# Optimization experiments

Measured on AMD Instinct MI355X. Metric: run time of the kernel, lower is better.

The kernel has to match this reference:

```python
import jax, jax.numpy as jnp
import numpy as np

B, NA, NB = 2, 2048, 2048
DIM_A, DIM_B = 256, 256
HEADS, DH_A, DH_B = 8, 64, 64
INNER_A, INNER_B = DH_A * HEADS, DH_B * HEADS
EPS = 1e-5


def layer_norm(x, w, b):
    m = jnp.mean(x, axis=-1, keepdims=True)
    v = jnp.mean(jnp.square(x - m), axis=-1, keepdims=True)
    return (x - m) * jax.lax.rsqrt(v + EPS) * w + b


def setup_inputs() -> dict:
    key = jax.random.key(0)
    ks = jax.random.split(key, 16)
    s = 0.02
    return {
        "feat_a": jax.random.normal(ks[0], (B, NA, DIM_A), jnp.float32),
        "feat_b": jax.random.normal(ks[1], (B, NB, DIM_B), jnp.float32),
        "mask_a_b": jax.random.bernoulli(ks[2], 0.5, (B, NA, NB)),
        # linear weights stored (in, out)
        "Wq": jax.random.normal(ks[3], (DIM_A, INNER_B), jnp.float32) * s,
        "bq": jnp.zeros((INNER_B,), jnp.float32),
        "Wk": jax.random.normal(ks[4], (DIM_B, INNER_B), jnp.float32) * s,
        "bk": jnp.zeros((INNER_B,), jnp.float32),
        "Wv": jax.random.normal(ks[5], (DIM_B, INNER_A), jnp.float32) * s,
        "bv": jnp.zeros((INNER_A,), jnp.float32),
        "Wg": jax.random.normal(ks[6], (DIM_A, INNER_A), jnp.float32) * s,
        "bg": jnp.zeros((INNER_A,), jnp.float32),
        "Wo": jax.random.normal(ks[7], (INNER_A, DIM_A), jnp.float32) * s,
        "bo": jnp.zeros((DIM_A,), jnp.float32),
        "ln_a_w": jnp.ones((DIM_A,), jnp.float32),
        "ln_a_b": jnp.zeros((DIM_A,), jnp.float32),
        "ln_b_w": jnp.ones((DIM_B,), jnp.float32),
        "ln_b_b": jnp.zeros((DIM_B,), jnp.float32),
        "qln_w": jnp.ones((INNER_B,), jnp.float32),
        "qln_b": jnp.zeros((INNER_B,), jnp.float32),
        "kln_w": jnp.ones((INNER_B,), jnp.float32),
        "kln_b": jnp.zeros((INNER_B,), jnp.float32),
    }


def reference(feat_a, feat_b, mask_a_b, Wq, bq, Wk, bk, Wv, bv, Wg, bg, Wo, bo,
              ln_a_w, ln_a_b, ln_b_w, ln_b_b, qln_w, qln_b, kln_w, kln_b):
    scale = DH_B ** -0.5
    fa = layer_norm(feat_a, ln_a_w, ln_a_b)            # (b, na, dim_a)
    fb = layer_norm(feat_b, ln_b_w, ln_b_b)            # (b, nb, dim_b)
    q = layer_norm(fa @ Wq + bq, qln_w, qln_b)         # (b, na, inner_b)
    k = layer_norm(fb @ Wk + bk, kln_w, kln_b)         # (b, nb, inner_b)
    v = fb @ Wv + bv                                   # (b, nb, inner_a)
    g = fa @ Wg + bg                                   # (b, na, inner_a)
    q = q.reshape(B, NA, HEADS, DH_B)
    k = k.reshape(B, NB, HEADS, DH_B)
    v = v.reshape(B, NB, HEADS, DH_A)
    g = g.reshape(B, NA, HEADS, DH_A)
    sim = jnp.einsum('bihd,bjhd->bhij', q, k) * scale  # (b, h, na, nb)
    neg = jnp.finfo(sim.dtype).min
    sim = jnp.where(mask_a_b[:, None, :, :], sim, neg)
    attn = jax.nn.softmax(sim, axis=-1)
    out = jnp.einsum('bhij,bjhd->bihd', attn, v)       # (b, na, h, dh_a)
    out = jax.nn.sigmoid(g) * out
    out = out.reshape(B, NA, INNER_A)
    return out @ Wo + bo                               # (b, na, dim_a)
```

## Files before the change

kernel.cpp:

```cpp
#include <hip/hip_runtime.h>
#include <hip/hip_bf16.h>

using bf16 = __hip_bfloat16;
typedef short bf16x8 __attribute__((ext_vector_type(8)));
typedef float f32x4 __attribute__((ext_vector_type(4)));
typedef unsigned short ushort8_t __attribute__((ext_vector_type(8)));
typedef unsigned long long u64;

static constexpr int NA_ = 2048, NB_ = 2048;
static constexpr int H_ = 8, DH_ = 64, INNER_ = 512;
static constexpr int MROWS = 2 * NA_;

#define MFMA32(a, b, c) __builtin_amdgcn_mfma_f32_16x16x32_bf16(a, b, c, 0, 0, 0)

__device__ __forceinline__ unsigned short bfbits(float x) {
  bf16 h = __float2bfloat16(x);
  return __builtin_bit_cast(unsigned short, h);
}
__device__ __forceinline__ float b2f(unsigned short u) {
  unsigned v = ((unsigned)u) << 16;
  return __builtin_bit_cast(float, v);
}

__global__ __launch_bounds__(256) void prep_kernel(
    const float* __restrict__ fa_in, const float* __restrict__ fb_in,
    const float* __restrict__ law, const float* __restrict__ lab,
    const float* __restrict__ lbw, const float* __restrict__ lbb,
    bf16* __restrict__ fa, bf16* __restrict__ fb,
    const float* __restrict__ Wq, const float* __restrict__ Wk,
    const float* __restrict__ Wv, const float* __restrict__ Wg,
    const float* __restrict__ Wo,
    bf16* __restrict__ Wqt, bf16* __restrict__ Wkt,
    bf16* __restrict__ Wvt, bf16* __restrict__ Wgt,
    bf16* __restrict__ Woth, bf16* __restrict__ Wotl,
    const void* __restrict__ maskp, u64* __restrict__ mbits) {
  int blk = blockIdx.x;
  int t = threadIdx.x;
  if (blk < 2048) {
    int row = blk * 4 + (t >> 6);
    int lane = t & 63;
    const float *src, *w, *bb;
    bf16* dst;
    int r;
    if (row < MROWS) { src = fa_in; w = law; bb = lab; dst = fa; r = row; }
    else             { src = fb_in; w = lbw; bb = lbb; dst = fb; r = row - MROWS; }
    float4 x = *(const float4*)(src + (size_t)r * 256 + lane * 4);
    float s  = (x.x + x.y) + (x.z + x.w);
    float s2 = (x.x * x.x + x.y * x.y) + (x.z * x.z + x.w * x.w);
#pragma unroll
    for (int m = 32; m >= 1; m >>= 1) { s += __shfl_xor(s, m); s2 += __shfl_xor(s2, m); }
    float mean = s * (1.0f / 256.0f);
    float var  = s2 * (1.0f / 256.0f) - mean * mean;
    float rstd = rsqrtf(var + 1e-5f);
    float4 wv = *(const float4*)(w + lane * 4);
    float4 bv = *(const float4*)(bb + lane * 4);
    ushort4 o;
    o.x = bfbits((x.x - mean) * rstd * wv.x + bv.x);
    o.y = bfbits((x.y - mean) * rstd * wv.y + bv.y);
    o.z = bfbits((x.z - mean) * rstd * wv.z + bv.z);
    o.w = bfbits((x.w - mean) * rstd * wv.w + bv.w);
    *(ushort4*)(dst + (size_t)r * 256 + lane * 4) = o;
  } else if (blk < 4608) {
    int z = (blk - 2048) >> 9;
    int idx = ((blk - 2048) & 511) * 256 + t;
    if (z < 4) {
      const float* W = (z == 0) ? Wq : (z == 1) ? Wk : (z == 2) ? Wv : Wg;
      bf16* Wt = (z == 0) ? Wqt : (z == 1) ? Wkt : (z == 2) ? Wvt : Wgt;
      int kk = idx >> 9, n = idx & 511;
      Wt[n * 256 + kk] = __float2bfloat16(W[idx]);
    } else {
      int kk = idx >> 8, n = idx & 255;
      float w = Wo[idx];
      bf16 hi = __float2bfloat16(w);
      Woth[n * 512 + kk] = hi;
      Wotl[n * 512 + kk] = __float2bfloat16(w - __bfloat162float(hi));
    }
  } else {
    __shared__ unsigned shf[4];
    const unsigned char* mu = (const unsigned char*)maskp;
    bool nz = ((t & 3) != 0) && (mu[t] != 0);
    u64 bal = __ballot(nz);
    if ((t & 63) == 0) shf[t >> 6] = (bal != 0ull) ? 1u : 0u;
    __syncthreads();
    bool m8 = (shf[0] | shf[1] | shf[2] | shf[3]) != 0;
    int lane = t & 63, wid = t >> 6;
    int lb = blk - 4608;
    for (size_t word = (size_t)lb * 4 + wid; word < 131072; word += 8192) {
      size_t e = word * 64 + lane;
      int v = m8 ? (int)mu[e] : ((const int*)maskp)[e];
      u64 b2 = __ballot(v != 0);
      if (lane == 0) mbits[word] = b2;
    }
  }
}

__global__ __launch_bounds__(256) void gemm4_kernel(
    const bf16* __restrict__ fa, const bf16* __restrict__ fb,
    const bf16* __restrict__ Wqt, const bf16* __restrict__ Wkt,
    const bf16* __restrict__ Wgt, const bf16* __restrict__ Wvt,
    const float* __restrict__ bq, const float* __restrict__ bk,
    const float* __restrict__ bg, const float* __restrict__ bv,
    const float* __restrict__ qlw, const float* __restrict__ qlb,
    const float* __restrict__ klw, const float* __restrict__ klb,
    bf16* __restrict__ qo, bf16* __restrict__ ko,
    bf16* __restrict__ gout, bf16* __restrict__ vout) {
  __shared__ __align__(16) char sm[27648];
  int z = blockIdx.z;
  int t = threadIdx.x, wave = t >> 6, lane = t & 63;
  int lm = lane & 15, quad = lane >> 4, q8 = quad * 8;

  if (z < 2) {
    bf16* As = (bf16*)sm;
    float* Pred = (float*)(sm + 16896);
    float* MV   = (float*)(sm + 17408);
    const bf16* A    = z ? fb : fa;
    const bf16* Wt   = z ? Wkt : Wqt;
    const float* bias = z ? bk : bq;
    const float* lw  = z ? klw : qlw;
    const float* lb  = z ? klb : qlb;
    bf16* out        = z ? ko : qo;
    int m0 = blockIdx.x * 16;
#pragma unroll
    for (int i = 0; i < 2; i++) {
      int id = t + 256 * i, r = id >> 5, cg = id & 31;
      *(ushort8_t*)(&As[r * 264 + cg * 8]) =
          *(const ushort8_t*)(A + (size_t)(m0 + r) * 256 + cg * 8);
    }
    __syncthreads();
    int n0w = wave * 128;
    f32x4 acc[8] = {};
    const bf16* wrow[8];
#pragma unroll
    for (int ni = 0; ni < 8; ni++) wrow[ni] = Wt + (size_t)(n0w + ni * 16 + lm) * 256;
#pragma unroll
    for (int ks = 0; ks < 8; ks++) {
      int k0 = ks * 32;
      bf16x8 af = *(const bf16x8*)(&As[lm * 264 + k0 + q8]);
#pragma unroll
      for (int ni = 0; ni < 8; ni++) {
        bf16x8 bf_ = *(const bf16x8*)(wrow[ni] + k0 + q8);
        acc[ni] = MFMA32(af, bf_, acc[ni]);
      }
    }
    float bvv[8];
#pragma unroll
    for (int ni = 0; ni < 8; ni++) bvv[ni] = bias[n0w + ni * 16 + lm];
#pragma unroll
    for (int ni = 0; ni < 8; ni++)
#pragma unroll
      for (int r = 0; r < 4; r++) acc[ni][r] += bvv[ni];
#pragma unroll
    for (int r = 0; r < 4; r++) {
      float s = 0.f, s2 = 0.f;
#pragma unroll
      for (int ni = 0; ni < 8; ni++) { s += acc[ni][r]; s2 += acc[ni][r] * acc[ni][r]; }
#pragma unroll
      for (int m = 1; m <= 8; m <<= 1) { s += __shfl_xor(s, m); s2 += __shfl_xor(s2, m); }
      if (lm == 0) {
        int row = quad * 4 + r;
        Pred[row * 8 + wave * 2]     = s;
        Pred[row * 8 + wave * 2 + 1] = s2;
      }
    }
    __syncthreads();
    if (t < 16) {
      float s = 0.f, s2 = 0.f;
#pragma unroll
      for (int w = 0; w < 4; w++) { s += Pred[t * 8 + w * 2]; s2 += Pred[t * 8 + w * 2 + 1]; }
      float mean = s * (1.0f / 512.0f);
      float var  = s2 * (1.0f / 512.0f) - mean * mean;
      MV[t * 2]     = mean;
      MV[t * 2 + 1] = rsqrtf(var + 1e-5f);
    }
    __syncthreads();
    float lww[8], lbb_[8];
#pragma unroll
    for (int ni = 0; ni < 8; ni++) {
      lww[ni]  = lw[n0w + ni * 16 + lm];
      lbb_[ni] = lb[n0w + ni * 16 + lm];
    }
#pragma unroll
    for (int r = 0; r < 4; r++) {
      int row = quad * 4 + r;
      float mean = MV[row * 2], rstd = MV[row * 2 + 1];
      size_t obase = (size_t)(m0 + row) * 512 + n0w;
#pragma unroll
      for (int ni = 0; ni < 8; ni++)
        out[obase + ni * 16 + lm] =
            __float2bfloat16((acc[ni][r] - mean) * rstd * lww[ni] + lbb_[ni]);
    }
  } else {
    bf16* As = (bf16*)sm;
    bf16* Bs = (bf16*)(sm + 18432);
    const bf16* A    = (z == 3) ? fb : fa;
    const bf16* Wt   = (z == 3) ? Wvt : Wgt;
    const float* bias = (z == 3) ? bv : bg;
    int x = blockIdx.x;
    int m0 = (x >> 3) * 128, n0 = (x & 7) * 64;
    int wm = wave * 32;
    f32x4 acc[2][4] = {};
    for (int k0 = 0; k0 < 256; k0 += 64) {
      __syncthreads();
#pragma unroll
      for (int i = 0; i < 4; i++) {
        int id = t + 256 * i, r = id >> 3, cg = id & 7;
        *(ushort8_t*)(&As[r * 72 + cg * 8]) =
            *(const ushort8_t*)(A + (size_t)(m0 + r) * 256 + k0 + cg * 8);
      }
#pragma unroll
      for (int i = 0; i < 2; i++) {
        int id = t + 256 * i, r = id >> 3, cg = id & 7;
        *(ushort8_t*)(&Bs[r * 72 + cg * 8]) =
            *(const ushort8_t*)(Wt + (size_t)(n0 + r) * 256 + k0 + cg * 8);
      }
      __syncthreads();
#pragma unroll
      for (int kk = 0; kk < 64; kk += 32) {
        bf16x8 af[2], bf_[4];
#pragma unroll
        for (int mi = 0; mi < 2; mi++)
          af[mi] = *(const bf16x8*)(&As[(wm + mi * 16 + lm) * 72 + kk + q8]);
#pragma unroll
        for (int ni = 0; ni < 4; ni++)
          bf_[ni] = *(const bf16x8*)(&Bs[(ni * 16 + lm) * 72 + kk + q8]);
#pragma unroll
        for (int mi = 0; mi < 2; mi++)
#pragma unroll
          for (int ni = 0; ni < 4; ni++)
            acc[mi][ni] = MFMA32(af[mi], bf_[ni], acc[mi][ni]);
      }
    }
    if (z == 2) {
#pragma unroll
      for (int mi = 0; mi < 2; mi++)
#pragma unroll
        for (int ni = 0; ni < 4; ni++) {
          int nn = n0 + ni * 16 + lm;
          float bvv = bias[nn];
          int mb = m0 + wm + mi * 16 + quad * 4;
#pragma unroll
          for (int r = 0; r < 4; r++)
            gout[(size_t)(mb + r) * 512 + nn] = __float2bfloat16(acc[mi][ni][r] + bvv);
        }
    } else {
      __syncthreads();
      bf16* buf = (bf16*)sm;
#pragma unroll
      for (int mi = 0; mi < 2; mi++)
#pragma unroll
        for (int ni = 0; ni < 4; ni++) {
          int d_local = ni * 16 + lm;
          float bvv = bias[n0 + d_local];
          int j_local = wm + mi * 16 + quad * 4;
#pragma unroll
          for (int r = 0; r < 4; r++)
            buf[d_local * 136 + j_local + r] = __float2bfloat16(acc[mi][ni][r] + bvv);
        }
      __syncthreads();
      int bidx2 = m0 >> 11, j0g = m0 & 2047, hh = n0 >> 6;
      int dl = t >> 2, jseg = (t & 3) * 32;
      bf16* dstrow = vout + (size_t)((bidx2 * 8 + hh) * 64 + dl) * 2048 + j0g + jseg;
#pragma unroll
      for (int c = 0; c < 4; c++)
        *(ushort8_t*)(dstrow + c * 8) = *(const ushort8_t*)(&buf[dl * 136 + jseg + c * 8]);
    }
  }
}

__global__ __launch_bounds__(512) void attn_kernel(
    const bf16* __restrict__ q, const bf16* __restrict__ k,
    const bf16* __restrict__ vt, const bf16* __restrict__ g,
    const u64* __restrict__ mbits,
    bf16* __restrict__ gh, bf16* __restrict__ gl) {
  __shared__ __align__(16) char smem[65024];
  bf16* Qs = (bf16*)smem;
  bf16* KsB = (bf16*)(smem + 9216);
  bf16* VsB = (bf16*)(smem + 27648);
  bf16* PsB = (bf16*)(smem + 46080);
  float* Om = (float*)(smem + 9216);
  float* Lbuf = (float*)(smem + 64512);

  int qt = blockIdx.x, bh = blockIdx.y;
  int bidx = bh >> 3, h = bh & 7;
  int i0 = qt * 64;
  int t = threadIdx.x, wave = t >> 6, lane = t & 63;
  int jhalf = wave >> 2, w4 = wave & 3;
  int lm = lane & 15, quad = lane >> 4, q8 = quad * 8;
  int lt = t & 255;
  int sr0 = lt >> 3, scg = (lt & 7) * 8;

  {
    int r = t >> 3, cg = t & 7;
    *(ushort8_t*)(&Qs[r * 72 + cg * 8]) =
        *(const ushort8_t*)(q + (size_t)(bidx * NA_ + i0 + r) * INNER_ + h * DH_ + cg * 8);
  }
  __syncthreads();
  bf16x8 bq0 = *(const bf16x8*)(&Qs[(w4 * 16 + lm) * 72 + q8]);
  bf16x8 bq1 = *(const bf16x8*)(&Qs[(w4 * 16 + lm) * 72 + 32 + q8]);

  f32x4 oacc[4] = {};
  float psum = 0.f;
  const float scale2 = 0.125f * 1.44269504088896f;

  const bf16* kb = k + (size_t)(bidx * NB_) * INNER_ + h * DH_;
  const bf16* vb = vt + (size_t)(bh * DH_) * NB_;
  bf16* Pw = PsB + wave * (16 * 72);
  bf16* Ks = KsB + jhalf * (64 * 72);
  bf16* Vs = VsB + jhalf * (64 * 72);
  const u64* mrp = mbits + ((size_t)(bidx * NA_ + i0 + w4 * 16 + lm)) * (NB_ / 64) + jhalf * 16;

  const bf16* ksrc0 = kb + (size_t)(jhalf * 1024 + sr0) * INNER_ + scg;
  const bf16* ksrc1 = kb + (size_t)(jhalf * 1024 + sr0 + 32) * INNER_ + scg;
  const bf16* vsrc0 = vb + (size_t)sr0 * NB_ + jhalf * 1024 + scg;
  const bf16* vsrc1 = vb + (size_t)(sr0 + 32) * NB_ + jhalf * 1024 + scg;

  ushort8_t kr0, kr1, vr0, vr1;
  kr0 = *(const ushort8_t*)(ksrc0);
  kr1 = *(const ushort8_t*)(ksrc1);
  vr0 = *(const ushort8_t*)(vsrc0);
  vr1 = *(const ushort8_t*)(vsrc1);
  u64 smw = mrp[0] >> (quad * 4);

  for (int it = 0; it < 16; it++) {
    __syncthreads();
    *(ushort8_t*)(&Ks[sr0 * 72 + scg])        = kr0;
    *(ushort8_t*)(&Ks[(sr0 + 32) * 72 + scg]) = kr1;
    *(ushort8_t*)(&Vs[sr0 * 72 + scg])        = vr0;
    *(ushort8_t*)(&Vs[(sr0 + 32) * 72 + scg]) = vr1;
    __syncthreads();

    u64 nsm = smw;
    if (it < 15) {
      int joff = (it + 1) * 64;
      kr0 = *(const ushort8_t*)(ksrc0 + (size_t)joff * INNER_);
      kr1 = *(const ushort8_t*)(ksrc1 + (size_t)joff * INNER_);
      vr0 = *(const ushort8_t*)(vsrc0 + joff);
      vr1 = *(const ushort8_t*)(vsrc1 + joff);
      nsm = mrp[it + 1] >> (quad * 4);
    }

    f32x4 st[4];
#pragma unroll
    for (int nt = 0; nt < 4; nt++) {
      bf16x8 a0 = *(const bf16x8*)(&Ks[(nt * 16 + lm) * 72 + q8]);
      bf16x8 a1 = *(const bf16x8*)(&Ks[(nt * 16 + lm) * 72 + 32 + q8]);
      f32x4 a = {0.f, 0.f, 0.f, 0.f};
      a = MFMA32(a0, bq0, a);
      a = MFMA32(a1, bq1, a);
      st[nt] = a;
    }

    float pr[4][4];
#pragma unroll
    for (int nt = 0; nt < 4; nt++)
#pragma unroll
      for (int r = 0; r < 4; r++) {
        float p = exp2f(st[nt][r] * scale2);
        unsigned live = (unsigned)(smw >> (nt * 16 + r)) & 1u;
        pr[nt][r] = live ? p : 0.0f;
      }

    float s0 = (pr[0][0] + pr[0][1]) + (pr[0][2] + pr[0][3]);
    float s1 = (pr[1][0] + pr[1][1]) + (pr[1][2] + pr[1][3]);
    float s2 = (pr[2][0] + pr[2][1]) + (pr[2][2] + pr[2][3]);
    float s3 = (pr[3][0] + pr[3][1]) + (pr[3][2] + pr[3][3]);
    psum += (s0 + s1) + (s2 + s3);

#pragma unroll
    for (int nt = 0; nt < 4; nt++) {
      ushort4 pk;
      pk.x = bfbits(pr[nt][0]);
      pk.y = bfbits(pr[nt][1]);
      pk.z = bfbits(pr[nt][2]);
      pk.w = bfbits(pr[nt][3]);
      *(ushort4*)(Pw + lm * 72 + nt * 16 + quad * 4) = pk;
    }

    bf16x8 ap0 = *(const bf16x8*)(&Pw[lm * 72 + q8]);
    bf16x8 ap1 = *(const bf16x8*)(&Pw[lm * 72 + 32 + q8]);
#pragma unroll
    for (int c = 0; c < 4; c++) {
      bf16x8 v0 = *(const bf16x8*)(&Vs[(c * 16 + lm) * 72 + q8]);
      bf16x8 v1 = *(const bf16x8*)(&Vs[(c * 16 + lm) * 72 + 32 + q8]);
      oacc[c] = MFMA32(ap0, v0, oacc[c]);
      oacc[c] = MFMA32(ap1, v1, oacc[c]);
    }
    smw = nsm;
  }

  psum += __shfl_xor(psum, 16);
  psum += __shfl_xor(psum, 32);

  __syncthreads();
  if (quad == 0) Lbuf[jhalf * 64 + w4 * 16 + lm] = psum;
  if (jhalf == 1) {
#pragma unroll
    for (int c = 0; c < 4; c++)
#pragma unroll
      for (int r = 0; r < 4; r++)
        Om[w4 * (16 * 66) + (quad * 4 + r) * 66 + c * 16 + lm] = oacc[c][r];
  }
  __syncthreads();
  if (jhalf == 0) {
    int mrow = i0 + w4 * 16 + quad * 4;
    float inv[4];
#pragma unroll
    for (int r = 0; r < 4; r++) {
      float l = Lbuf[w4 * 16 + quad * 4 + r] + Lbuf[64 + w4 * 16 + quad * 4 + r];
      inv[r] = 1.0f / l;
    }
#pragma unroll
    for (int c = 0; c < 4; c++) {
      int col = h * DH_ + c * 16 + lm;
#pragma unroll
      for (int r = 0; r < 4; r++) {
        float o = oacc[c][r] + Om[w4 * (16 * 66) + (quad * 4 + r) * 66 + c * 16 + lm];
        size_t idx = (size_t)(bidx * NA_ + mrow + r) * INNER_ + col;
        float gv = b2f(__builtin_bit_cast(unsigned short, g[idx]));
        float sig = 1.0f / (1.0f + __expf(-gv));
        float val = o * inv[r] * sig;
        unsigned short hb = bfbits(val);
        gh[idx] = __builtin_bit_cast(bf16, hb);
        gl[idx] = __float2bfloat16(val - b2f(hb));
      }
    }
  }
}

__global__ __launch_bounds__(256) void gemm_split_kernel(
    const bf16* __restrict__ Ah, const bf16* __restrict__ Al,
    const bf16* __restrict__ Bh, const bf16* __restrict__ Bl,
    const float* __restrict__ bias, float* __restrict__ C) {
  constexpr int K = 512, N = 256;
  __shared__ __align__(16) bf16 Ash[32 * 72];
  __shared__ __align__(16) bf16 Asl[32 * 72];
  __shared__ __align__(16) bf16 Bsh[64 * 72];
  __shared__ __align__(16) bf16 Bsl[64 * 72];
  int n0 = blockIdx.x * 64, m0 = blockIdx.y * 32;
  int t = threadIdx.x, wave = t >> 6, lane = t & 63;
  int lm = lane & 15, quad = lane >> 4, q8 = quad * 8;
  int wm = (wave & 1) * 16, wn = (wave >> 1) * 32;
  f32x4 acc[2] = {};
  for (int k0 = 0; k0 < K; k0 += 64) {
    __syncthreads();
    {
      int r = t >> 3, cg = t & 7;
      size_t ga = (size_t)(m0 + r) * K + k0 + cg * 8;
      *(ushort8_t*)(&Ash[r * 72 + cg * 8]) = *(const ushort8_t*)(Ah + ga);
      *(ushort8_t*)(&Asl[r * 72 + cg * 8]) = *(const ushort8_t*)(Al + ga);
    }
#pragma unroll
    for (int i = 0; i < 2; i++) {
      int id = t + 256 * i, r = id >> 3, cg = id & 7;
      size_t gb = (size_t)(n0 + r) * K + k0 + cg * 8;
      *(ushort8_t*)(&Bsh[r * 72 + cg * 8]) = *(const ushort8_t*)(Bh + gb);
      *(ushort8_t*)(&Bsl[r * 72 + cg * 8]) = *(const ushort8_t*)(Bl + gb);
    }
    __syncthreads();
#pragma unroll
    for (int kk = 0; kk < 64; kk += 32) {
      bf16x8 ah = *(const bf16x8*)(&Ash[(wm + lm) * 72 + kk + q8]);
      bf16x8 al = *(const bf16x8*)(&Asl[(wm + lm) * 72 + kk + q8]);
#pragma unroll
      for (int ni = 0; ni < 2; ni++) {
        bf16x8 bh_ = *(const bf16x8*)(&Bsh[(wn + ni * 16 + lm) * 72 + kk + q8]);
        bf16x8 bl_ = *(const bf16x8*)(&Bsl[(wn + ni * 16 + lm) * 72 + kk + q8]);
        acc[ni] = MFMA32(ah, bh_, acc[ni]);
        acc[ni] = MFMA32(ah, bl_, acc[ni]);
        acc[ni] = MFMA32(al, bh_, acc[ni]);
      }
    }
  }
#pragma unroll
  for (int ni = 0; ni < 2; ni++) {
    int n = n0 + wn + ni * 16 + lm;
    float bvv = bias[n];
    int mb = m0 + wm + quad * 4;
#pragma unroll
    for (int r = 0; r < 4; r++) C[(size_t)(mb + r) * N + n] = acc[ni][r] + bvv;
  }
}

extern "C" void kernel_launch(void* const* d_in, const int* in_sizes, int n_in,
                              void* d_out, int out_size, void* d_ws, size_t ws_size,
                              hipStream_t stream) {
  const float* feat_a = (const float*)d_in[0];
  const float* feat_b = (const float*)d_in[1];
  const void*  mask   = d_in[2];
  const float* Wq = (const float*)d_in[3];
  const float* bq = (const float*)d_in[4];
  const float* Wk = (const float*)d_in[5];
  const float* bk = (const float*)d_in[6];
  const float* Wv = (const float*)d_in[7];
  const float* bv = (const float*)d_in[8];
  const float* Wg = (const float*)d_in[9];
  const float* bg = (const float*)d_in[10];
  const float* Wo = (const float*)d_in[11];
  const float* bo = (const float*)d_in[12];
  const float* law = (const float*)d_in[13];
  const float* lab = (const float*)d_in[14];
  const float* lbw = (const float*)d_in[15];
  const float* lbb = (const float*)d_in[16];
  const float* qlw = (const float*)d_in[17];
  const float* qlb = (const float*)d_in[18];
  const float* klw = (const float*)d_in[19];
  const float* klb = (const float*)d_in[20];

  char* ws = (char*)d_ws;
  size_t off = 0;
  auto alloc = [&](size_t bytes) -> void* {
    void* p = ws + off;
    off += (bytes + 255) & ~(size_t)255;
    return p;
  };
  bf16* fa    = (bf16*)alloc((size_t)MROWS * 256 * 2);
  bf16* fb    = (bf16*)alloc((size_t)MROWS * 256 * 2);
  bf16* Wqt   = (bf16*)alloc((size_t)131072 * 2);
  bf16* Wkt   = (bf16*)alloc((size_t)131072 * 2);
  bf16* Wvt   = (bf16*)alloc((size_t)131072 * 2);
  bf16* Wgt   = (bf16*)alloc((size_t)131072 * 2);
  bf16* Woth  = (bf16*)alloc((size_t)131072 * 2);
  bf16* Wotl  = (bf16*)alloc((size_t)131072 * 2);
  bf16* qb_   = (bf16*)alloc((size_t)MROWS * 512 * 2);
  bf16* kb_   = (bf16*)alloc((size_t)MROWS * 512 * 2);
  bf16* vtb   = (bf16*)alloc((size_t)1024 * 2048 * 2);
  bf16* gbuf  = (bf16*)alloc((size_t)MROWS * 512 * 2);
  bf16* gh    = (bf16*)alloc((size_t)MROWS * 512 * 2);
  bf16* gl    = (bf16*)alloc((size_t)MROWS * 512 * 2);
  u64*  mbits = (u64*)alloc((size_t)131072 * 8);

  prep_kernel<<<6656, 256, 0, stream>>>(
      feat_a, feat_b, law, lab, lbw, lbb, fa, fb,
      Wq, Wk, Wv, Wg, Wo, Wqt, Wkt, Wvt, Wgt, Woth, Wotl, mask, mbits);
  gemm4_kernel<<<dim3(256, 1, 4), 256, 0, stream>>>(
      fa, fb, Wqt, Wkt, Wgt, Wvt, bq, bk, bg, bv,
      qlw, qlb, klw, klb, qb_, kb_, gbuf, vtb);
  attn_kernel<<<dim3(32, 16), 512, 0, stream>>>(qb_, kb_, vtb, gbuf, mbits, gh, gl);
  gemm_split_kernel<<<dim3(4, 128), 256, 0, stream>>>(gh, gl, Woth, Wotl, bo, (float*)d_out);
}
```

Measured before the change: 202.1 us.

## Fold softmax scale into q LayerNorm and compute row sums via MFMA

Folds the attention scale and log2e factor into the q LayerNorm weight and bias, which removes a multiply per score. Masked scores are set to -200 before a raw hardware exp2, replacing the exp-then-select sequence. Probabilities are packed to bf16 with an add-and-permute round instead of the library conversion. Row sums now come from an extra pair of MFMAs against a ones vector rather than scalar adds and shuffles. The row sums now use bf16-rounded probabilities, and pkbf's simplified rounding (ties not handled to even) differs slightly from the library conversion.

```diff
diff --git a/kernel.cpp b/kernel.cpp
--- a/kernel.cpp
+++ b/kernel.cpp
@@ -13,6 +13,12 @@
 
 #define MFMA32(a, b, c) __builtin_amdgcn_mfma_f32_16x16x32_bf16(a, b, c, 0, 0, 0)
 
+#if __has_builtin(__builtin_amdgcn_exp2f)
+#define EXP2(x) __builtin_amdgcn_exp2f(x)
+#else
+#define EXP2(x) exp2f(x)
+#endif
+
 __device__ __forceinline__ unsigned short bfbits(float x) {
   bf16 h = __float2bfloat16(x);
   return __builtin_bit_cast(unsigned short, h);
@@ -20,6 +26,16 @@
 __device__ __forceinline__ float b2f(unsigned short u) {
   unsigned v = ((unsigned)u) << 16;
   return __builtin_bit_cast(float, v);
+}
+
+__device__ __forceinline__ unsigned pkbf(float a, float b) {
+  unsigned ua = __builtin_bit_cast(unsigned, a) + 0x8000u;
+  unsigned ub = __builtin_bit_cast(unsigned, b) + 0x8000u;
+#if __has_builtin(__builtin_amdgcn_perm)
+  return __builtin_amdgcn_perm(ub, ua, 0x07060302u);
+#else
+  return (ua >> 16) | (ub & 0xFFFF0000u);
+#endif
 }
 
 __global__ __launch_bounds__(256) void prep_kernel(
@@ -179,6 +195,11 @@
       lww[ni]  = lw[n0w + ni * 16 + lm];
       lbb_[ni] = lb[n0w + ni * 16 + lm];
     }
+    if (z == 0) {
+      const float SC = 0.125f * 1.44269504088896f;
+#pragma unroll
+      for (int ni = 0; ni < 8; ni++) { lww[ni] *= SC; lbb_[ni] *= SC; }
+    }
 #pragma unroll
     for (int r = 0; r < 4; r++) {
       int row = quad * 4 + r;
@@ -298,9 +319,15 @@
   bf16x8 bq0 = *(const bf16x8*)(&Qs[(w4 * 16 + lm) * 72 + q8]);
   bf16x8 bq1 = *(const bf16x8*)(&Qs[(w4 * 16 + lm) * 72 + 32 + q8]);
 
+  bf16x8 bone;
+  {
+    short onev = (lm == 0) ? (short)0x3F80 : (short)0;
+#pragma unroll
+    for (int i = 0; i < 8; i++) bone[i] = onev;
+  }
+
   f32x4 oacc[4] = {};
-  float psum = 0.f;
-  const float scale2 = 0.125f * 1.44269504088896f;
+  f32x4 lacc = {};
 
   const bf16* kb = k + (size_t)(bidx * NB_) * INNER_ + h * DH_;
   const bf16* vb = vt + (size_t)(bh * DH_) * NB_;
@@ -355,25 +382,17 @@
     for (int nt = 0; nt < 4; nt++)
 #pragma unroll
       for (int r = 0; r < 4; r++) {
-        float p = exp2f(st[nt][r] * scale2);
-        unsigned live = (unsigned)(smw >> (nt * 16 + r)) & 1u;
-        pr[nt][r] = live ? p : 0.0f;
-      }
-
-    float s0 = (pr[0][0] + pr[0][1]) + (pr[0][2] + pr[0][3]);
-    float s1 = (pr[1][0] + pr[1][1]) + (pr[1][2] + pr[1][3]);
-    float s2 = (pr[2][0] + pr[2][1]) + (pr[2][2] + pr[2][3]);
-    float s3 = (pr[3][0] + pr[3][1]) + (pr[3][2] + pr[3][3]);
-    psum += (s0 + s1) + (s2 + s3);
+        bool live = (smw >> (nt * 16 + r)) & 1ull;
+        float sv = live ? st[nt][r] : -200.0f;
+        pr[nt][r] = EXP2(sv);
+      }
 
 #pragma unroll
     for (int nt = 0; nt < 4; nt++) {
-      ushort4 pk;
-      pk.x = bfbits(pr[nt][0]);
-      pk.y = bfbits(pr[nt][1]);
-      pk.z = bfbits(pr[nt][2]);
-      pk.w = bfbits(pr[nt][3]);
-      *(ushort4*)(Pw + lm * 72 + nt * 16 + quad * 4) = pk;
+      uint2 pk;
+      pk.x = pkbf(pr[nt][0], pr[nt][1]);
+      pk.y = pkbf(pr[nt][2], pr[nt][3]);
+      *(uint2*)(Pw + lm * 72 + nt * 16 + quad * 4) = pk;
     }
 
     bf16x8 ap0 = *(const bf16x8*)(&Pw[lm * 72 + q8]);
@@ -385,14 +404,18 @@
       oacc[c] = MFMA32(ap0, v0, oacc[c]);
       oacc[c] = MFMA32(ap1, v1, oacc[c]);
     }
+    lacc = MFMA32(ap0, bone, lacc);
+    lacc = MFMA32(ap1, bone, lacc);
+
     smw = nsm;
   }
 
-  psum += __shfl_xor(psum, 16);
-  psum += __shfl_xor(psum, 32);
-
   __syncthreads();
-  if (quad == 0) Lbuf[jhalf * 64 + w4 * 16 + lm] = psum;
+  if (lm == 0) {
+#pragma unroll
+    for (int r = 0; r < 4; r++)
+      Lbuf[jhalf * 64 + w4 * 16 + quad * 4 + r] = lacc[r];
+  }
   if (jhalf == 1) {
 #pragma unroll
     for (int c = 0; c < 4; c++)
```

Measured after the change: 200.6 us. Within noise of the previous version (-0.7%).
